# Kernel tuning notes

Measured on AMD Instinct MI355X. Metric: run time of the kernel, lower is better.

The kernel has to match this reference:

```python
import jax, jax.numpy as jnp
import numpy as np

N_NODES = 50000
N_EDGES = 800000
D_FEAT = 128
HIDDEN = 128
BERT_DIM = 768
BATCH = 4096
MAX_ENT = 20
COMB = BERT_DIM + HIDDEN  # 896


def setup_inputs() -> dict:
    key = jax.random.key(0)
    ks = jax.random.split(key, 12)
    article_bert_embeddings = jax.random.normal(ks[0], (BATCH, BERT_DIM), dtype=jnp.float32)
    x = jax.random.normal(ks[1], (N_NODES, D_FEAT), dtype=jnp.float32)
    edge_index = jax.random.randint(ks[2], (2, N_EDGES), 0, N_NODES, dtype=jnp.int64)
    entity_map = jax.random.randint(ks[3], (BATCH, MAX_ENT), 0, N_NODES, dtype=jnp.int64)
    pad = jax.random.uniform(ks[4], (BATCH, MAX_ENT)) < 0.3
    entity_map = jnp.where(pad, jnp.int64(-1), entity_map)
    s = 1.0 / np.sqrt(D_FEAT)
    W1 = jax.random.normal(ks[5], (D_FEAT, HIDDEN), dtype=jnp.float32) * s
    b1 = jnp.zeros((HIDDEN,), dtype=jnp.float32)
    W2 = jax.random.normal(ks[6], (HIDDEN, HIDDEN), dtype=jnp.float32) * (1.0 / np.sqrt(HIDDEN))
    b2 = jnp.zeros((HIDDEN,), dtype=jnp.float32)
    fc1_w = jax.random.normal(ks[7], (COMB, COMB // 2), dtype=jnp.float32) * (1.0 / np.sqrt(COMB))
    fc1_b = jnp.zeros((COMB // 2,), dtype=jnp.float32)
    fc2_w = jax.random.normal(ks[8], (COMB // 2, 1), dtype=jnp.float32) * (1.0 / np.sqrt(COMB // 2))
    fc2_b = jnp.zeros((1,), dtype=jnp.float32)
    return dict(article_bert_embeddings=article_bert_embeddings, x=x,
                edge_index=edge_index, entity_map=entity_map,
                W1=W1, b1=b1, W2=W2, b2=b2,
                fc1_w=fc1_w, fc1_b=fc1_b, fc2_w=fc2_w, fc2_b=fc2_b)


def _gcn_norm(edge_index, n_nodes):
    # add self loops (PyG GCNConv default) and compute symmetric normalization
    loops = jnp.arange(n_nodes, dtype=edge_index.dtype)
    src = jnp.concatenate([edge_index[0], loops])
    dst = jnp.concatenate([edge_index[1], loops])
    deg = jax.ops.segment_sum(jnp.ones_like(dst, dtype=jnp.float32), dst, num_segments=n_nodes)
    dinv = jnp.where(deg > 0, jax.lax.rsqrt(deg), 0.0)
    norm = dinv[src] * dinv[dst]  # [E+N]
    return src, dst, norm


def _gcn_conv(h, W, b, src, dst, norm, n_nodes):
    h = h @ W                                   # [N, H] transform first (cheaper)
    msg = h[src] * norm[:, None]                # [E+N, H] gather
    out = jax.ops.segment_sum(msg, dst, num_segments=n_nodes)
    return out + b


def reference(article_bert_embeddings, x, edge_index, entity_map,
              W1, b1, W2, b2, fc1_w, fc1_b, fc2_w, fc2_b):
    n = x.shape[0]
    src, dst, norm = _gcn_norm(edge_index, n)
    # GNN (dropout in eval mode = identity)
    h = jax.nn.relu(_gcn_conv(x, W1, b1, src, dst, norm, n))
    h = jax.nn.relu(_gcn_conv(h, W2, b2, src, dst, norm, n))
    # ragged mean over entity lists (-1 = padding), fully vectorized
    mask = entity_map >= 0                           # [B, M]
    safe_ids = jnp.where(mask, entity_map, 0)
    gathered = h[safe_ids] * mask[..., None]         # [B, M, H]
    cnt = jnp.maximum(mask.sum(axis=1, keepdims=True).astype(h.dtype), 1.0)
    batch_gnn = gathered.sum(axis=1) / cnt           # [B, H]; rows w/ no entities stay 0
    combined = jnp.concatenate([article_bert_embeddings, batch_gnn], axis=1)
    z = jax.nn.relu(combined @ fc1_w + fc1_b)
    logits = z @ fc2_w + fc2_b
    return jax.nn.sigmoid(logits)
```

## Files before the change

### kernel.cpp

```cpp
#include <hip/hip_runtime.h>
#include <math.h>

typedef __bf16 bf16_t;
typedef __bf16 bfrag8 __attribute__((ext_vector_type(8)));
typedef float  facc4  __attribute__((ext_vector_type(4)));
typedef float  f32x2  __attribute__((ext_vector_type(2)));

#define NBUCK 512
#define BCAP  4096
#define BINCH 2048

__device__ inline unsigned short f2b(float x) {
    unsigned int u = __float_as_uint(x);
    unsigned int r = (u + 0x7fffu + ((u >> 16) & 1u)) >> 16;
    return (unsigned short)r;
}
__device__ inline unsigned int pack2(float lo, float hi) {
    return (unsigned int)f2b(lo) | ((unsigned int)f2b(hi) << 16);
}
__device__ inline float blo(unsigned int q) { return __uint_as_float(q << 16); }
__device__ inline float bhi(unsigned int q) { return __uint_as_float(q & 0xffff0000u); }

#if __has_builtin(__builtin_amdgcn_cvt_pk_f32_fp8) && __has_builtin(__builtin_amdgcn_cvt_pk_fp8_f32)
#define HW_FP8 1
#endif

__device__ inline f32x2 fp8pair_dec(unsigned short v) {
#ifdef HW_FP8
    return __builtin_amdgcn_cvt_pk_f32_fp8((int)(unsigned int)v, false);
#else
    f32x2 r;
    unsigned char b0 = (unsigned char)(v & 0xff), b1 = (unsigned char)(v >> 8);
    {
        int e = (b0 >> 3) & 0xf, m = b0 & 7;
        float mag = e ? ldexpf(8.f + m, e - 10) : ldexpf((float)m, -9);
        r.x = (b0 & 0x80) ? -mag : mag;
    }
    {
        int e = (b1 >> 3) & 0xf, m = b1 & 7;
        float mag = e ? ldexpf(8.f + m, e - 10) : ldexpf((float)m, -9);
        r.y = (b1 & 0x80) ? -mag : mag;
    }
    return r;
#endif
}
__device__ inline unsigned char fp8_enc(float x) {
#ifdef HW_FP8
    return (unsigned char)(__builtin_amdgcn_cvt_pk_fp8_f32(x, x, 0, false) & 0xff);
#else
    unsigned char s = (x < 0.f) ? 0x80 : 0;
    float ax = fabsf(x);
    if (!(ax > 0.f)) return s;
    if (ax >= 448.f) return s | 0x7e;
    if (ax < 0.015625f) {
        int q = (int)rintf(ax * 512.f);
        return s | (unsigned char)q;
    }
    int e; float m = frexpf(ax, &e);
    int q = (int)rintf(m * 16.f);
    int E = e - 1;
    if (q == 16) { q = 8; ++E; }
    if (E > 8) return s | 0x7e;
    return s | (unsigned char)(((E + 7) << 3) | (q - 8));
#endif
}

__device__ inline int bucket_of(int d, int N) {
    return (int)(((long long)d * NBUCK) / N);
}


__device__ inline void bin2_body(char* smem, const int* __restrict__ src,
                                 const int* __restrict__ dst,
                                 int* __restrict__ bcnt,
                                 unsigned int* __restrict__ ebuf,
                                 int E, int N, int bb) {
    unsigned int* sorted = (unsigned int*)smem;
    int* hist   = (int*)(smem + 16384);
    int* lstart = (int*)(smem + 18432);
    int* gbase  = (int*)(smem + 20480);
    int* sm     = (int*)(smem + 22528);
    int tid = threadIdx.x;
    int base = bb * BINCH;
    int cnt = min(BINCH, E - base);
    hist[tid] = 0; hist[tid + 256] = 0;
    __syncthreads();
    unsigned int mye[8]; int myb[8];
#pragma unroll
    for (int i = 0; i < 8; ++i) {
        int idx = i * 256 + tid;
        myb[i] = -1;
        if (idx < cnt) {
            int e = base + idx;
            int s = src[e], d = dst[e];
            mye[i] = ((unsigned int)s << 16) | (unsigned int)d;
            int b = bucket_of(d, N);
            myb[i] = b;
            atomicAdd(&hist[b], 1);
        }
    }
    __syncthreads();
    int p0 = hist[2 * tid], p1 = hist[2 * tid + 1];
    sm[tid] = p0 + p1;
    __syncthreads();
    for (int off = 1; off < 256; off <<= 1) {
        int x = (tid >= off) ? sm[tid - off] : 0;
        __syncthreads();
        sm[tid] += x;
        __syncthreads();
    }
    int excl = sm[tid] - (p0 + p1);
    lstart[2 * tid] = excl;
    lstart[2 * tid + 1] = excl + p0;
    __syncthreads();
    hist[tid] = lstart[tid]; hist[tid + 256] = lstart[tid + 256];
    __syncthreads();
#pragma unroll
    for (int i = 0; i < 8; ++i) {
        if (myb[i] >= 0) {
            int pos = atomicAdd(&hist[myb[i]], 1);
            sorted[pos] = mye[i];
        }
    }
    __syncthreads();
    for (int b = tid; b < NBUCK; b += 256) {
        int c = hist[b] - lstart[b];
        gbase[b] = (c > 0) ? atomicAdd(&bcnt[b], c) : 0;
    }
    __syncthreads();
    for (int idx = tid; idx < cnt; idx += 256) {
        unsigned int v = sorted[idx];
        int b = bucket_of((int)(v & 0xffffu), N);
        ebuf[(size_t)b * BCAP + gbase[b] + (idx - lstart[b])] = v;
    }
}

__device__ inline void build2_body(char* smem, const unsigned int* __restrict__ ebuf,
                                   const int* __restrict__ bcnt,
                                   int* __restrict__ offs,
                                   float* __restrict__ dinv,
                                   unsigned short* __restrict__ csr,
                                   int N, int E, int b) {
    unsigned short* seg = (unsigned short*)smem;
    int* cnt_l  = (int*)(smem + 8192);
    int* scan_l = (int*)(smem + 8704);
    int* curs   = (int*)(smem + 9216);
    int* smr    = (int*)(smem + 9728);
    int tid = threadIdx.x;
    int part = 0;
    for (int j = tid; j < b; j += 256) part += bcnt[j];
    smr[tid] = part;
    __syncthreads();
    for (int off = 128; off > 0; off >>= 1) {
        if (tid < off) smr[tid] += smr[tid + off];
        __syncthreads();
    }
    int base = smr[0];
    int lo = (int)(((long long)b * N + NBUCK - 1) / NBUCK);
    int cnt = bcnt[b];
    int nrange = (int)(((long long)(b + 1) * N + NBUCK - 1) / NBUCK) - lo;
    if (b == 0 && tid == 0) offs[N] = E;
    if (tid < 128) cnt_l[tid] = 0;
    __syncthreads();
    for (int i = tid; i < cnt; i += 256) {
        unsigned int v = ebuf[(size_t)b * BCAP + i];
        atomicAdd(&cnt_l[(int)(v & 0xffffu) - lo], 1);
    }
    __syncthreads();
    if (tid < 128) scan_l[tid] = cnt_l[tid];
    __syncthreads();
    for (int off = 1; off < 128; off <<= 1) {
        int x = 0;
        if (tid < 128 && tid >= off) x = scan_l[tid - off];
        __syncthreads();
        if (tid < 128) scan_l[tid] += x;
        __syncthreads();
    }
    if (tid < 128) {
        int excl = scan_l[tid] - cnt_l[tid];
        curs[tid] = excl;
        if (tid < nrange) {
            offs[lo + tid] = base + excl;
            dinv[lo + tid] = rsqrtf((float)(cnt_l[tid] + 1));
        }
    }
    __syncthreads();
    for (int i = tid; i < cnt; i += 256) {
        unsigned int v = ebuf[(size_t)b * BCAP + i];
        int d = (int)(v & 0xffffu) - lo;
        int p = atomicAdd(&curs[d], 1);
        seg[p] = (unsigned short)(v >> 16);
    }
    __syncthreads();
    for (int i = tid; i < cnt; i += 256) csr[base + i] = seg[i];
}

__device__ inline void gemm1_body(char* smem, const float* __restrict__ A,
                                  const bf16_t* __restrict__ Bt,
                                  unsigned char* __restrict__ out8, int M, int bb) {
    bf16_t* As = (bf16_t*)smem;
    bf16_t* Bs = (bf16_t*)(smem + 17408);
    int t = threadIdx.x;
    int wave = t >> 6, lane = t & 63, quad = lane >> 4, l16 = lane & 15;
    int r0 = bb * 64;
#pragma unroll
    for (int i = 0; i < 4; ++i) {
        int chunk = t + i * 256;
        int row = chunk >> 4, c8 = (chunk & 15) << 3;
        int gr = r0 + row;
        float4 a0 = make_float4(0.f, 0.f, 0.f, 0.f), a1 = a0;
        if (gr < M) {
            a0 = *(const float4*)&A[(size_t)gr * 128 + c8];
            a1 = *(const float4*)&A[(size_t)gr * 128 + c8 + 4];
        }
        *(uint4*)&As[row * 136 + c8] =
            make_uint4(pack2(a0.x, a0.y), pack2(a0.z, a0.w),
                       pack2(a1.x, a1.y), pack2(a1.z, a1.w));
    }
#pragma unroll
    for (int i = 0; i < 8; ++i) {
        int chunk = t + i * 256;
        int row = chunk >> 4, c8 = (chunk & 15) << 3;
        *(uint4*)&Bs[row * 136 + c8] = *(const uint4*)&Bt[row * 128 + c8];
    }
    __syncthreads();

    facc4 acc[8];
#pragma unroll
    for (int nt = 0; nt < 8; ++nt) acc[nt] = (facc4){0.f, 0.f, 0.f, 0.f};
    int arow = (wave << 4) + l16;
#pragma unroll
    for (int ks = 0; ks < 4; ++ks) {
        int kk = ks * 32 + quad * 8;
        bfrag8 af = *(const bfrag8*)&As[arow * 136 + kk];
#pragma unroll
        for (int nt = 0; nt < 8; ++nt) {
            bfrag8 bf = *(const bfrag8*)&Bs[(nt * 16 + l16) * 136 + kk];
            acc[nt] = __builtin_amdgcn_mfma_f32_16x16x32_bf16(af, bf, acc[nt], 0, 0, 0);
        }
    }
    __syncthreads();
    unsigned char* f8t = (unsigned char*)As;
    int wrow0 = (wave << 4) + quad * 4;
#pragma unroll
    for (int r = 0; r < 4; ++r) {
        int row = wrow0 + r;
#pragma unroll
        for (int nt = 0; nt < 8; ++nt)
            f8t[row * 128 + nt * 16 + l16] = fp8_enc(acc[nt][r]);
    }
    __syncthreads();
#pragma unroll
    for (int i = 0; i < 2; ++i) {
        int idx = t + i * 256;
        int row = idx >> 3, cc = (idx & 7) << 4;
        int gr = r0 + row;
        if (gr < M) *(uint4*)&out8[(size_t)gr * 128 + cc] = *(const uint4*)&f8t[row * 128 + cc];
    }
}

__global__ __launch_bounds__(256) void k_bin_gemm(const int* __restrict__ src,
                                                  const int* __restrict__ dst,
                                                  int* __restrict__ bcnt,
                                                  unsigned int* __restrict__ ebuf,
                                                  int E, int N,
                                                  const float* __restrict__ A,
                                                  const bf16_t* __restrict__ Bt,
                                                  unsigned char* __restrict__ out8,
                                                  int nbin) {
    __shared__ __align__(16) char smem[52224];
    if ((int)blockIdx.x < nbin)
        bin2_body(smem, src, dst, bcnt, ebuf, E, N, blockIdx.x);
    else
        gemm1_body(smem, A, Bt, out8, N, blockIdx.x - nbin);
}

__global__ __launch_bounds__(256) void k_build_gemm(const unsigned int* __restrict__ ebuf,
                                                    const int* __restrict__ bcnt,
                                                    int* __restrict__ offs,
                                                    float* __restrict__ dinv,
                                                    unsigned short* __restrict__ csr,
                                                    int N, int E,
                                                    const float* __restrict__ A,
                                                    const bf16_t* __restrict__ Bt,
                                                    unsigned char* __restrict__ out8,
                                                    int tile0) {
    __shared__ __align__(16) char smem[52224];
    if ((int)blockIdx.x < NBUCK)
        build2_body(smem, ebuf, bcnt, offs, dinv, csr, N, E, blockIdx.x);
    else
        gemm1_body(smem, A, Bt, out8, N, blockIdx.x - NBUCK + tile0);
}

__global__ __launch_bounds__(256) void k_prep(const float* __restrict__ bert,
                                              unsigned int* __restrict__ bertb, int n8,
                                              const float* __restrict__ W1,
                                              unsigned short* __restrict__ w1t,
                                              const float* __restrict__ W2,
                                              unsigned short* __restrict__ w2t,
                                              const float* __restrict__ Wf,
                                              unsigned short* __restrict__ fwt,
                                              int* __restrict__ bcnt,
                                              float* __restrict__ logacc) {
    __shared__ float tile[64][65];
    int ncvt = (n8 + 255) / 256;
    int bb = blockIdx.x, tid = threadIdx.x;
    if (bb < ncvt) {
        int i = bb * 256 + tid;
        if (i >= n8) return;
        const float4* p = (const float4*)bert + (size_t)i * 2;
        float4 a = p[0], b = p[1];
        uint4 o;
        o.x = pack2(a.x, a.y);
        o.y = pack2(a.z, a.w);
        o.z = pack2(b.x, b.y);
        o.w = pack2(b.z, b.w);
        ((uint4*)bertb)[i] = o;
        return;
    }
    bb -= ncvt;
    if (bb < 128) {
        int i = bb * 256 + tid;
        const float* W = (i < 16384) ? W1 : W2;
        unsigned short* Wt = (i < 16384) ? w1t : w2t;
        int idx = i & 16383;
        int n = idx >> 7, k = idx & 127;
        Wt[idx] = f2b(W[k * 128 + n]);
        return;
    }
    bb -= 128;
    if (bb < 98) {
        int n0 = (bb % 7) * 64, k0 = (bb / 7) * 64;
#pragma unroll
        for (int i = 0; i < 16; ++i) {
            int idx = i * 256 + tid;
            int r = idx >> 6, c = idx & 63;
            tile[r][c] = Wf[(size_t)(k0 + r) * 448 + n0 + c];
        }
        __syncthreads();
#pragma unroll
        for (int i = 0; i < 16; ++i) {
            int idx = i * 256 + tid;
            int c = idx >> 6, r = idx & 63;
            fwt[(size_t)(n0 + c) * 896 + k0 + r] = f2b(tile[r][c]);
        }
        return;
    }
    if (tid < 256) { bcnt[tid] = 0; bcnt[tid + 256] = 0; }
#pragma unroll
    for (int i = 0; i < 16; ++i) logacc[i * 256 + tid] = 0.f;
}

__global__ __launch_bounds__(256) void k_gemm_nn128(const bf16_t* __restrict__ A,
                                                    const bf16_t* __restrict__ Bt,
                                                    const float* __restrict__ rs,
                                                    unsigned char* __restrict__ out8, int M) {
    __shared__ bf16_t As[64 * 136];
    __shared__ bf16_t Bs[128 * 136];
    int t = threadIdx.x;
    int wave = t >> 6, lane = t & 63, quad = lane >> 4, l16 = lane & 15;
    int r0 = blockIdx.x * 64;
#pragma unroll
    for (int i = 0; i < 4; ++i) {
        int chunk = t + i * 256;
        int row = chunk >> 4, c8 = (chunk & 15) << 3;
        int gr = r0 + row;
        uint4 v = make_uint4(0u, 0u, 0u, 0u);
        if (gr < M) v = *(const uint4*)&A[(size_t)gr * 128 + c8];
        *(uint4*)&As[row * 136 + c8] = v;
    }
#pragma unroll
    for (int i = 0; i < 8; ++i) {
        int chunk = t + i * 256;
        int row = chunk >> 4, c8 = (chunk & 15) << 3;
        *(uint4*)&Bs[row * 136 + c8] = *(const uint4*)&Bt[row * 128 + c8];
    }
    __syncthreads();

    facc4 acc[8];
#pragma unroll
    for (int nt = 0; nt < 8; ++nt) acc[nt] = (facc4){0.f, 0.f, 0.f, 0.f};
    int arow = (wave << 4) + l16;
#pragma unroll
    for (int ks = 0; ks < 4; ++ks) {
        int kk = ks * 32 + quad * 8;
        bfrag8 af = *(const bfrag8*)&As[arow * 136 + kk];
#pragma unroll
        for (int nt = 0; nt < 8; ++nt) {
            bfrag8 bf = *(const bfrag8*)&Bs[(nt * 16 + l16) * 136 + kk];
            acc[nt] = __builtin_amdgcn_mfma_f32_16x16x32_bf16(af, bf, acc[nt], 0, 0, 0);
        }
    }
    __syncthreads();
    unsigned char* f8t = (unsigned char*)As;
    int wrow0 = (wave << 4) + quad * 4;
#pragma unroll
    for (int r = 0; r < 4; ++r) {
        int row = wrow0 + r;
        float sc = rs[min(r0 + row, M - 1)];
#pragma unroll
        for (int nt = 0; nt < 8; ++nt)
            f8t[row * 128 + nt * 16 + l16] = fp8_enc(acc[nt][r] * sc);
    }
    __syncthreads();
#pragma unroll
    for (int i = 0; i < 2; ++i) {
        int idx = t + i * 256;
        int row = idx >> 3, cc = (idx & 7) << 4;
        int gr = r0 + row;
        if (gr < M) *(uint4*)&out8[(size_t)gr * 128 + cc] = *(const uint4*)&f8t[row * 128 + cc];
    }
}

__global__ __launch_bounds__(256) void k_agg_w(const unsigned short* __restrict__ hx8,
                                               const unsigned short* __restrict__ csr,
                                               const int* __restrict__ offs,
                                               const float* __restrict__ dinv,
                                               const float* __restrict__ bias,
                                               unsigned int* __restrict__ out, int N) {
    int node = blockIdx.x * 4 + (threadIdx.x >> 6);
    int lane = threadIdx.x & 63;
    if (node >= N) return;
    float di = dinv[node];
    f32x2 sf = fp8pair_dec(hx8[(size_t)node * 64 + lane]);
    float acc0 = sf.x * di, acc1 = sf.y * di;
    int s0 = offs[node], s1 = offs[node + 1];
    for (int base = s0; base < s1; base += 64) {
        int nloc = min(64, s1 - base);
        int en = 0; float dvl = 0.f;
        if (lane < nloc) { en = (int)csr[base + lane]; dvl = dinv[en]; }
        int j = 0;
        for (; j + 16 <= nloc; j += 16) {
            int sid[16]; float dv[16]; unsigned short g[16];
#pragma unroll
            for (int u = 0; u < 16; ++u) {
                sid[u] = __shfl(en, j + u, 64);
                dv[u]  = __shfl(dvl, j + u, 64);
            }
#pragma unroll
            for (int u = 0; u < 16; ++u) g[u] = hx8[(size_t)sid[u] * 64 + lane];
#pragma unroll
            for (int u = 0; u < 16; ++u) {
                f32x2 d = fp8pair_dec(g[u]);
                acc0 += d.x * dv[u]; acc1 += d.y * dv[u];
            }
        }
        for (; j + 4 <= nloc; j += 4) {
            int sid[4]; float dv[4]; unsigned short g[4];
#pragma unroll
            for (int u = 0; u < 4; ++u) {
                sid[u] = __shfl(en, j + u, 64);
                dv[u]  = __shfl(dvl, j + u, 64);
            }
#pragma unroll
            for (int u = 0; u < 4; ++u) g[u] = hx8[(size_t)sid[u] * 64 + lane];
#pragma unroll
            for (int u = 0; u < 4; ++u) {
                f32x2 d = fp8pair_dec(g[u]);
                acc0 += d.x * dv[u]; acc1 += d.y * dv[u];
            }
        }
        for (; j < nloc; ++j) {
            int srcn = __shfl(en, j, 64);
            float dv = __shfl(dvl, j, 64);
            f32x2 d = fp8pair_dec(hx8[(size_t)srcn * 64 + lane]);
            acc0 += d.x * dv; acc1 += d.y * dv;
        }
    }
    float2 bb = *(const float2*)&bias[lane * 2];
    float v0 = fmaxf(acc0 * di + bb.x, 0.f);
    float v1 = fmaxf(acc1 * di + bb.y, 0.f);
    out[(size_t)node * 64 + lane] = pack2(v0, v1);
}

__global__ __launch_bounds__(256) void k_agg_b(const unsigned short* __restrict__ hx8,
                                               const unsigned short* __restrict__ csr,
                                               const int* __restrict__ offs,
                                               const float* __restrict__ dinv,
                                               const float* __restrict__ bias,
                                               unsigned int* __restrict__ out, int N) {
    int node = blockIdx.x * 4 + (threadIdx.x >> 6);
    int lane = threadIdx.x & 63;
    if (node >= N) return;
    float di = dinv[node];
    f32x2 sf = fp8pair_dec(hx8[(size_t)node * 64 + lane]);
    float acc0 = sf.x, acc1 = sf.y;
    int s0 = offs[node], s1 = offs[node + 1];
    for (int base = s0; base < s1; base += 64) {
        int nloc = min(64, s1 - base);
        int en = 0;
        if (lane < nloc) en = (int)csr[base + lane];
        int j = 0;
        for (; j + 16 <= nloc; j += 16) {
            int sid[16]; unsigned short g[16];
#pragma unroll
            for (int u = 0; u < 16; ++u) sid[u] = __shfl(en, j + u, 64);
#pragma unroll
            for (int u = 0; u < 16; ++u) g[u] = hx8[(size_t)sid[u] * 64 + lane];
#pragma unroll
            for (int u = 0; u < 16; ++u) { f32x2 d = fp8pair_dec(g[u]); acc0 += d.x; acc1 += d.y; }
        }
        for (; j + 4 <= nloc; j += 4) {
            int sid[4]; unsigned short g[4];
#pragma unroll
            for (int u = 0; u < 4; ++u) sid[u] = __shfl(en, j + u, 64);
#pragma unroll
            for (int u = 0; u < 4; ++u) g[u] = hx8[(size_t)sid[u] * 64 + lane];
#pragma unroll
            for (int u = 0; u < 4; ++u) { f32x2 d = fp8pair_dec(g[u]); acc0 += d.x; acc1 += d.y; }
        }
        for (; j < nloc; ++j) {
            int srcn = __shfl(en, j, 64);
            f32x2 d = fp8pair_dec(hx8[(size_t)srcn * 64 + lane]);
            acc0 += d.x; acc1 += d.y;
        }
    }
    float2 bb = *(const float2*)&bias[lane * 2];
    float v0 = fmaxf(acc0 * di + bb.x, 0.f);
    float v1 = fmaxf(acc1 * di + bb.y, 0.f);
    out[(size_t)node * 64 + lane] = pack2(v0, v1);
}

__global__ __launch_bounds__(256) void k_pool_b(const unsigned int* __restrict__ h,
                                                const int* __restrict__ ent,
                                                unsigned int* __restrict__ out) {
    int r = blockIdx.x * 4 + (threadIdx.x >> 6);
    int lane = threadIdx.x & 63;
    float a0 = 0.f, a1 = 0.f;
    int cnt = 0;
#pragma unroll
    for (int m = 0; m < 20; ++m) {
        int id = ent[r * 20 + m];
        if (id >= 0) {
            unsigned int q = h[(size_t)id * 64 + lane];
            a0 += blo(q); a1 += bhi(q); cnt++;
        }
    }
    float inv = 1.f / (float)max(cnt, 1);
    out[(size_t)r * 64 + lane] = pack2(a0 * inv, a1 * inv);
}

__global__ __launch_bounds__(256) void k_mlp1_mfma(const bf16_t* __restrict__ bertb,
                                                   const bf16_t* __restrict__ gnnb,
                                                   const bf16_t* __restrict__ fwt,
                                                   const float* __restrict__ fb,
                                                   const float* __restrict__ w2,
                                                   float* __restrict__ logacc) {
    __shared__ bf16_t As[64 * 136];
    __shared__ bf16_t Bs[64 * 136];
    int t = threadIdx.x;
    int wave = t >> 6, lane = t & 63, quad = lane >> 4, l16 = lane & 15;
    int r0 = blockIdx.x * 64, c0 = blockIdx.y * 64;
    facc4 acc[4];
#pragma unroll
    for (int nt = 0; nt < 4; ++nt) acc[nt] = (facc4){0.f, 0.f, 0.f, 0.f};

    for (int ks = 0; ks < 7; ++ks) {
#pragma unroll
        for (int i = 0; i < 4; ++i) {
            int chunk = t + i * 256;
            int row = chunk >> 4, c8 = (chunk & 15) << 3;
            int gr = r0 + row;
            const bf16_t* srcp = (ks < 6) ? &bertb[(size_t)gr * 768 + ks * 128 + c8]
                                          : &gnnb[(size_t)gr * 128 + c8];
            *(uint4*)&As[row * 136 + c8] = *(const uint4*)srcp;
        }
#pragma unroll
        for (int i = 0; i < 4; ++i) {
            int chunk = t + i * 256;
            int row = chunk >> 4, c8 = (chunk & 15) << 3;
            *(uint4*)&Bs[row * 136 + c8] =
                *(const uint4*)&fwt[(size_t)(c0 + row) * 896 + ks * 128 + c8];
        }
        __syncthreads();
        int arow = (wave << 4) + l16;
#pragma unroll
        for (int sub = 0; sub < 4; ++sub) {
            int kk = sub * 32 + quad * 8;
            bfrag8 af = *(const bfrag8*)&As[arow * 136 + kk];
#pragma unroll
            for (int nt = 0; nt < 4; ++nt) {
                bfrag8 bf = *(const bfrag8*)&Bs[(nt * 16 + l16) * 136 + kk];
                acc[nt] = __builtin_amdgcn_mfma_f32_16x16x32_bf16(af, bf, acc[nt], 0, 0, 0);
            }
        }
        __syncthreads();
    }
    int rbase = r0 + (wave << 4) + quad * 4;
    float part[4] = {0.f, 0.f, 0.f, 0.f};
#pragma unroll
    for (int nt = 0; nt < 4; ++nt) {
        int col = c0 + nt * 16 + l16;
        float bb = fb[col];
        float ww = w2[col];
#pragma unroll
        for (int r = 0; r < 4; ++r)
            part[r] += fmaxf(acc[nt][r] + bb, 0.f) * ww;
    }
#pragma unroll
    for (int m = 8; m >= 1; m >>= 1) {
#pragma unroll
        for (int r = 0; r < 4; ++r) part[r] += __shfl_xor(part[r], m, 64);
    }
    if (l16 == 0) {
#pragma unroll
        for (int r = 0; r < 4; ++r) atomicAdd(&logacc[rbase + r], part[r]);
    }
}

__global__ void k_sig(const float* __restrict__ logacc, const float* __restrict__ b,
                      float* __restrict__ out, int B) {
    int i = blockIdx.x * 256 + threadIdx.x;
    if (i < B) out[i] = 1.f / (1.f + expf(-(logacc[i] + b[0])));
}

extern "C" void kernel_launch(void* const* d_in, const int* in_sizes, int n_in,
                              void* d_out, int out_size, void* d_ws, size_t ws_size,
                              hipStream_t stream) {
    const float* bert = (const float*)d_in[0];
    const float* x    = (const float*)d_in[1];
    const int*   ei   = (const int*)d_in[2];
    const int*   ent  = (const int*)d_in[3];
    const float* W1   = (const float*)d_in[4];
    const float* b1   = (const float*)d_in[5];
    const float* W2   = (const float*)d_in[6];
    const float* b2   = (const float*)d_in[7];
    const float* fc1w = (const float*)d_in[8];
    const float* fc1b = (const float*)d_in[9];
    const float* fc2w = (const float*)d_in[10];
    const float* fc2b = (const float*)d_in[11];
    float* out = (float*)d_out;

    const int N = in_sizes[1] / 128;
    const int E = in_sizes[2] / 2;
    const int B = in_sizes[0] / 768;

    const int* srcv = ei;
    const int* dstv = ei + E;

    char* wsp = (char*)d_ws;
    size_t off = 0;
    auto alloc = [&](size_t bytes) -> void* {
        void* p = wsp + off;
        off += (bytes + 255) & ~(size_t)255;
        return p;
    };
    float* dinv   = (float*)alloc((size_t)N * 4);
    int*   offs   = (int*)alloc((size_t)(N + 1) * 4);
    int*   bcnt   = (int*)alloc(NBUCK * 4);
    float* logacc = (float*)alloc((size_t)B * 4);
    unsigned int*   ebuf  = (unsigned int*)alloc((size_t)NBUCK * BCAP * 4);
    unsigned short* csr16 = (unsigned short*)alloc((size_t)E * 2);
    bf16_t* bertb = (bf16_t*)alloc((size_t)B * 768 * 2);
    bf16_t* w1t   = (bf16_t*)alloc(128 * 128 * 2);
    bf16_t* w2t   = (bf16_t*)alloc(128 * 128 * 2);
    bf16_t* fwt   = (bf16_t*)alloc((size_t)896 * 448 * 2);
    unsigned char* g8a = (unsigned char*)alloc((size_t)N * 128);
    unsigned char* g8b = (unsigned char*)alloc((size_t)N * 128);
    bf16_t* hbuf  = (bf16_t*)alloc((size_t)N * 128 * 2);
    bf16_t* gnnb  = (bf16_t*)alloc((size_t)B * 128 * 2);
    (void)ws_size; (void)n_in; (void)out_size;

    int nb8 = B * 768 / 8;
    int ncvt = (nb8 + 255) / 256;
    int nprep = ncvt + 128 + 98 + 1;
    int nbin = (E + BINCH - 1) / BINCH;
    int gb = (N + 63) / 64;
    int g1a = gb / 2, g1b = gb - g1a;

    k_prep<<<nprep, 256, 0, stream>>>(bert, (unsigned int*)bertb, nb8,
                                      W1, (unsigned short*)w1t, W2, (unsigned short*)w2t,
                                      fc1w, (unsigned short*)fwt, bcnt, logacc);
    k_bin_gemm<<<nbin + g1a, 256, 0, stream>>>(srcv, dstv, bcnt, ebuf, E, N,
                                               x, w1t, g8a, nbin);
    k_build_gemm<<<NBUCK + g1b, 256, 0, stream>>>(ebuf, bcnt, offs, dinv, csr16, N, E,
                                                  x, w1t, g8a, g1a);
    k_agg_w<<<(N + 3) / 4, 256, 0, stream>>>((const unsigned short*)g8a, csr16, offs, dinv, b1,
                                             (unsigned int*)hbuf, N);
    k_gemm_nn128<<<gb, 256, 0, stream>>>(hbuf, w2t, dinv, g8b, N);
    k_agg_b<<<(N + 3) / 4, 256, 0, stream>>>((const unsigned short*)g8b, csr16, offs, dinv, b2,
                                             (unsigned int*)hbuf, N);
    k_pool_b<<<B / 4, 256, 0, stream>>>((const unsigned int*)hbuf, ent, (unsigned int*)gnnb);
    k_mlp1_mfma<<<dim3(B / 64, 7), 256, 0, stream>>>(bertb, gnnb, fwt, fc1b, fc2w, logacc);
    k_sig<<<(B + 255) / 256, 256, 0, stream>>>(logacc, fc2b, out, B);
}
```

Before: 214.9 us.

## Process four nodes per wave in aggregation, prescale layer-1 features, halve GEMM LDS

Unifies the two aggregation kernels into one that handles four destination nodes per wave and interleaves their neighbor gathers to raise memory-level parallelism. Layer-1 source scaling by dinv moves into a separate pass that rewrites the fp8 features in place. The GEMMs now load the weight matrix in two 64-row halves, which cuts shared memory per block to allow higher occupancy. The changes add an extra kernel pass, a second fp8 rounding, and wasted iterations when the four nodes' degrees differ.

```diff
diff --git a/kernel.cpp b/kernel.cpp
--- a/kernel.cpp
+++ b/kernel.cpp
@@ -9,6 +9,7 @@
 #define NBUCK 512
 #define BCAP  4096
 #define BINCH 2048
+#define KN 4
 
 __device__ inline unsigned short f2b(float x) {
     unsigned int u = __float_as_uint(x);
@@ -217,37 +218,39 @@
             make_uint4(pack2(a0.x, a0.y), pack2(a0.z, a0.w),
                        pack2(a1.x, a1.y), pack2(a1.z, a1.w));
     }
-#pragma unroll
-    for (int i = 0; i < 8; ++i) {
-        int chunk = t + i * 256;
-        int row = chunk >> 4, c8 = (chunk & 15) << 3;
-        *(uint4*)&Bs[row * 136 + c8] = *(const uint4*)&Bt[row * 128 + c8];
-    }
-    __syncthreads();
-
     facc4 acc[8];
 #pragma unroll
     for (int nt = 0; nt < 8; ++nt) acc[nt] = (facc4){0.f, 0.f, 0.f, 0.f};
     int arow = (wave << 4) + l16;
 #pragma unroll
-    for (int ks = 0; ks < 4; ++ks) {
-        int kk = ks * 32 + quad * 8;
-        bfrag8 af = *(const bfrag8*)&As[arow * 136 + kk];
-#pragma unroll
-        for (int nt = 0; nt < 8; ++nt) {
-            bfrag8 bf = *(const bfrag8*)&Bs[(nt * 16 + l16) * 136 + kk];
-            acc[nt] = __builtin_amdgcn_mfma_f32_16x16x32_bf16(af, bf, acc[nt], 0, 0, 0);
-        }
-    }
-    __syncthreads();
+    for (int h = 0; h < 2; ++h) {
+#pragma unroll
+        for (int i = 0; i < 4; ++i) {
+            int chunk = t + i * 256;
+            int row = chunk >> 4, c8 = (chunk & 15) << 3;
+            *(uint4*)&Bs[row * 136 + c8] = *(const uint4*)&Bt[(h * 64 + row) * 128 + c8];
+        }
+        __syncthreads();
+#pragma unroll
+        for (int ks = 0; ks < 4; ++ks) {
+            int kk = ks * 32 + quad * 8;
+            bfrag8 af = *(const bfrag8*)&As[arow * 136 + kk];
+#pragma unroll
+            for (int nt = 0; nt < 4; ++nt) {
+                bfrag8 bf = *(const bfrag8*)&Bs[(nt * 16 + l16) * 136 + kk];
+                acc[h * 4 + nt] = __builtin_amdgcn_mfma_f32_16x16x32_bf16(af, bf, acc[h * 4 + nt], 0, 0, 0);
+            }
+        }
+        __syncthreads();
+    }
     unsigned char* f8t = (unsigned char*)As;
     int wrow0 = (wave << 4) + quad * 4;
 #pragma unroll
     for (int r = 0; r < 4; ++r) {
         int row = wrow0 + r;
 #pragma unroll
-        for (int nt = 0; nt < 8; ++nt)
-            f8t[row * 128 + nt * 16 + l16] = fp8_enc(acc[nt][r]);
+        for (int nt2 = 0; nt2 < 8; ++nt2)
+            f8t[row * 128 + (nt2 >> 2) * 64 + (nt2 & 3) * 16 + l16] = fp8_enc(acc[nt2][r]);
     }
     __syncthreads();
 #pragma unroll
@@ -268,7 +271,7 @@
                                                   const bf16_t* __restrict__ Bt,
                                                   unsigned char* __restrict__ out8,
                                                   int nbin) {
-    __shared__ __align__(16) char smem[52224];
+    __shared__ __align__(16) char smem[34816];
     if ((int)blockIdx.x < nbin)
         bin2_body(smem, src, dst, bcnt, ebuf, E, N, blockIdx.x);
     else
@@ -285,7 +288,7 @@
                                                     const bf16_t* __restrict__ Bt,
                                                     unsigned char* __restrict__ out8,
                                                     int tile0) {
-    __shared__ __align__(16) char smem[52224];
+    __shared__ __align__(16) char smem[34816];
     if ((int)blockIdx.x < NBUCK)
         build2_body(smem, ebuf, bcnt, offs, dinv, csr, N, E, blockIdx.x);
     else
@@ -351,12 +354,35 @@
     for (int i = 0; i < 16; ++i) logacc[i * 256 + tid] = 0.f;
 }
 
+__global__ __launch_bounds__(256) void k_scale8(unsigned int* __restrict__ g8,
+                                                const float* __restrict__ dinv, int N) {
+    int i = blockIdx.x * 256 + threadIdx.x;
+    int total = N * 8;
+    if (i >= total) return;
+    int row = i >> 3;
+    float d = dinv[row];
+    uint4 v = ((const uint4*)g8)[i];
+    unsigned int w[4] = {v.x, v.y, v.z, v.w};
+#pragma unroll
+    for (int q = 0; q < 4; ++q) {
+        unsigned int x = w[q], y = 0;
+#pragma unroll
+        for (int h = 0; h < 2; ++h) {
+            f32x2 p = fp8pair_dec((unsigned short)(x >> (h * 16)));
+            y |= (unsigned int)fp8_enc(p.x * d) << (h * 16);
+            y |= (unsigned int)fp8_enc(p.y * d) << (h * 16 + 8);
+        }
+        w[q] = y;
+    }
+    ((uint4*)g8)[i] = make_uint4(w[0], w[1], w[2], w[3]);
+}
+
 __global__ __launch_bounds__(256) void k_gemm_nn128(const bf16_t* __restrict__ A,
                                                     const bf16_t* __restrict__ Bt,
                                                     const float* __restrict__ rs,
                                                     unsigned char* __restrict__ out8, int M) {
     __shared__ bf16_t As[64 * 136];
-    __shared__ bf16_t Bs[128 * 136];
+    __shared__ bf16_t Bs[64 * 136];
     int t = threadIdx.x;
     int wave = t >> 6, lane = t & 63, quad = lane >> 4, l16 = lane & 15;
     int r0 = blockIdx.x * 64;
@@ -369,29 +395,31 @@
         if (gr < M) v = *(const uint4*)&A[(size_t)gr * 128 + c8];
         *(uint4*)&As[row * 136 + c8] = v;
     }
-#pragma unroll
-    for (int i = 0; i < 8; ++i) {
-        int chunk = t + i * 256;
-        int row = chunk >> 4, c8 = (chunk & 15) << 3;
-        *(uint4*)&Bs[row * 136 + c8] = *(const uint4*)&Bt[row * 128 + c8];
-    }
-    __syncthreads();
-
     facc4 acc[8];
 #pragma unroll
     for (int nt = 0; nt < 8; ++nt) acc[nt] = (facc4){0.f, 0.f, 0.f, 0.f};
     int arow = (wave << 4) + l16;
 #pragma unroll
-    for (int ks = 0; ks < 4; ++ks) {
-        int kk = ks * 32 + quad * 8;
-        bfrag8 af = *(const bfrag8*)&As[arow * 136 + kk];
-#pragma unroll
-        for (int nt = 0; nt < 8; ++nt) {
-            bfrag8 bf = *(const bfrag8*)&Bs[(nt * 16 + l16) * 136 + kk];
-            acc[nt] = __builtin_amdgcn_mfma_f32_16x16x32_bf16(af, bf, acc[nt], 0, 0, 0);
-        }
-    }
-    __syncthreads();
+    for (int h = 0; h < 2; ++h) {
+#pragma unroll
+        for (int i = 0; i < 4; ++i) {
+            int chunk = t + i * 256;
+            int row = chunk >> 4, c8 = (chunk & 15) << 3;
+            *(uint4*)&Bs[row * 136 + c8] = *(const uint4*)&Bt[(h * 64 + row) * 128 + c8];
+        }
+        __syncthreads();
+#pragma unroll
+        for (int ks = 0; ks < 4; ++ks) {
+            int kk = ks * 32 + quad * 8;
+            bfrag8 af = *(const bfrag8*)&As[arow * 136 + kk];
+#pragma unroll
+            for (int nt = 0; nt < 4; ++nt) {
+                bfrag8 bf = *(const bfrag8*)&Bs[(nt * 16 + l16) * 136 + kk];
+                acc[h * 4 + nt] = __builtin_amdgcn_mfma_f32_16x16x32_bf16(af, bf, acc[h * 4 + nt], 0, 0, 0);
+            }
+        }
+        __syncthreads();
+    }
     unsigned char* f8t = (unsigned char*)As;
     int wrow0 = (wave << 4) + quad * 4;
 #pragma unroll
@@ -399,8 +427,8 @@
         int row = wrow0 + r;
         float sc = rs[min(r0 + row, M - 1)];
 #pragma unroll
-        for (int nt = 0; nt < 8; ++nt)
-            f8t[row * 128 + nt * 16 + l16] = fp8_enc(acc[nt][r] * sc);
+        for (int nt2 = 0; nt2 < 8; ++nt2)
+            f8t[row * 128 + (nt2 >> 2) * 64 + (nt2 & 3) * 16 + l16] = fp8_enc(acc[nt2][r] * sc);
     }
     __syncthreads();
 #pragma unroll
@@ -412,113 +440,77 @@
     }
 }
 
-__global__ __launch_bounds__(256) void k_agg_w(const unsigned short* __restrict__ hx8,
+__global__ __launch_bounds__(256) void k_agg_p(const unsigned short* __restrict__ hx8,
                                                const unsigned short* __restrict__ csr,
                                                const int* __restrict__ offs,
                                                const float* __restrict__ dinv,
                                                const float* __restrict__ bias,
                                                unsigned int* __restrict__ out, int N) {
-    int node = blockIdx.x * 4 + (threadIdx.x >> 6);
-    int lane = threadIdx.x & 63;
-    if (node >= N) return;
-    float di = dinv[node];
-    f32x2 sf = fp8pair_dec(hx8[(size_t)node * 64 + lane]);
-    float acc0 = sf.x * di, acc1 = sf.y * di;
-    int s0 = offs[node], s1 = offs[node + 1];
-    for (int base = s0; base < s1; base += 64) {
-        int nloc = min(64, s1 - base);
-        int en = 0; float dvl = 0.f;
-        if (lane < nloc) { en = (int)csr[base + lane]; dvl = dinv[en]; }
-        int j = 0;
-        for (; j + 16 <= nloc; j += 16) {
-            int sid[16]; float dv[16]; unsigned short g[16];
-#pragma unroll
-            for (int u = 0; u < 16; ++u) {
-                sid[u] = __shfl(en, j + u, 64);
-                dv[u]  = __shfl(dvl, j + u, 64);
+    int t = threadIdx.x, wv = t >> 6, lane = t & 63;
+    int nb = (blockIdx.x * 4 + wv) * KN;
+    if (nb >= N) return;
+    float a0[KN], a1[KN], di[KN];
+    int s0[KN], dg[KN];
+#pragma unroll
+    for (int k = 0; k < KN; ++k) {
+        int nd = nb + k;
+        if (nd < N) {
+            f32x2 s = fp8pair_dec(hx8[(size_t)nd * 64 + lane]);
+            a0[k] = s.x; a1[k] = s.y;
+            s0[k] = offs[nd];
+            dg[k] = offs[nd + 1] - s0[k];
+            di[k] = dinv[nd];
+        } else { a0[k] = a1[k] = 0.f; s0[k] = 0; dg[k] = 0; di[k] = 0.f; }
+    }
+    int maxd = 0;
+#pragma unroll
+    for (int k = 0; k < KN; ++k) maxd = max(maxd, dg[k]);
+    for (int eb = 0; eb < maxd; eb += 64) {
+        int en[KN];
+#pragma unroll
+        for (int k = 0; k < KN; ++k) {
+            int nl = dg[k] - eb;
+            en[k] = 0;
+            if (nl > 0 && lane < nl) en[k] = (int)csr[s0[k] + eb + lane];
+        }
+        for (int j = 0; j < 64; j += 8) {
+            unsigned short g[KN][8];
+            bool any = false;
+#pragma unroll
+            for (int k = 0; k < KN; ++k) {
+                int nl = dg[k] - eb; if (nl > 64) nl = 64;
+                if (j < nl) {
+                    any = true;
+#pragma unroll
+                    for (int u = 0; u < 8; ++u) {
+                        int sid = __shfl(en[k], j + u, 64);
+                        g[k][u] = (j + u < nl) ? hx8[(size_t)sid * 64 + lane] : (unsigned short)0;
+                    }
+                } else {
+#pragma unroll
+                    for (int u = 0; u < 8; ++u) g[k][u] = 0;
+                }
             }
-#pragma unroll
-            for (int u = 0; u < 16; ++u) g[u] = hx8[(size_t)sid[u] * 64 + lane];
-#pragma unroll
-            for (int u = 0; u < 16; ++u) {
-                f32x2 d = fp8pair_dec(g[u]);
-                acc0 += d.x * dv[u]; acc1 += d.y * dv[u];
-            }
-        }
-        for (; j + 4 <= nloc; j += 4) {
-            int sid[4]; float dv[4]; unsigned short g[4];
-#pragma unroll
-            for (int u = 0; u < 4; ++u) {
-                sid[u] = __shfl(en, j + u, 64);
-                dv[u]  = __shfl(dvl, j + u, 64);
-            }
-#pragma unroll
-            for (int u = 0; u < 4; ++u) g[u] = hx8[(size_t)sid[u] * 64 + lane];
-#pragma unroll
-            for (int u = 0; u < 4; ++u) {
-                f32x2 d = fp8pair_dec(g[u]);
-                acc0 += d.x * dv[u]; acc1 += d.y * dv[u];
-            }
-        }
-        for (; j < nloc; ++j) {
-            int srcn = __shfl(en, j, 64);
-            float dv = __shfl(dvl, j, 64);
-            f32x2 d = fp8pair_dec(hx8[(size_t)srcn * 64 + lane]);
-            acc0 += d.x * dv; acc1 += d.y * dv;
+            if (!any) break;
+#pragma unroll
+            for (int k = 0; k < KN; ++k)
+#pragma unroll
+                for (int u = 0; u < 8; ++u) {
+                    f32x2 d = fp8pair_dec(g[k][u]);
+                    a0[k] += d.x; a1[k] += d.y;
+                }
         }
     }
     float2 bb = *(const float2*)&bias[lane * 2];
-    float v0 = fmaxf(acc0 * di + bb.x, 0.f);
-    float v1 = fmaxf(acc1 * di + bb.y, 0.f);
-    out[(size_t)node * 64 + lane] = pack2(v0, v1);
-}
-
-__global__ __launch_bounds__(256) void k_agg_b(const unsigned short* __restrict__ hx8,
-                                               const unsigned short* __restrict__ csr,
-                                               const int* __restrict__ offs,
-                                               const float* __restrict__ dinv,
-                                               const float* __restrict__ bias,
-                                               unsigned int* __restrict__ out, int N) {
-    int node = blockIdx.x * 4 + (threadIdx.x >> 6);
-    int lane = threadIdx.x & 63;
-    if (node >= N) return;
-    float di = dinv[node];
-    f32x2 sf = fp8pair_dec(hx8[(size_t)node * 64 + lane]);
-    float acc0 = sf.x, acc1 = sf.y;
-    int s0 = offs[node], s1 = offs[node + 1];
-    for (int base = s0; base < s1; base += 64) {
-        int nloc = min(64, s1 - base);
-        int en = 0;
-        if (lane < nloc) en = (int)csr[base + lane];
-        int j = 0;
-        for (; j + 16 <= nloc; j += 16) {
-            int sid[16]; unsigned short g[16];
-#pragma unroll
-            for (int u = 0; u < 16; ++u) sid[u] = __shfl(en, j + u, 64);
-#pragma unroll
-            for (int u = 0; u < 16; ++u) g[u] = hx8[(size_t)sid[u] * 64 + lane];
-#pragma unroll
-            for (int u = 0; u < 16; ++u) { f32x2 d = fp8pair_dec(g[u]); acc0 += d.x; acc1 += d.y; }
-        }
-        for (; j + 4 <= nloc; j += 4) {
-            int sid[4]; unsigned short g[4];
-#pragma unroll
-            for (int u = 0; u < 4; ++u) sid[u] = __shfl(en, j + u, 64);
-#pragma unroll
-            for (int u = 0; u < 4; ++u) g[u] = hx8[(size_t)sid[u] * 64 + lane];
-#pragma unroll
-            for (int u = 0; u < 4; ++u) { f32x2 d = fp8pair_dec(g[u]); acc0 += d.x; acc1 += d.y; }
-        }
-        for (; j < nloc; ++j) {
-            int srcn = __shfl(en, j, 64);
-            f32x2 d = fp8pair_dec(hx8[(size_t)srcn * 64 + lane]);
-            acc0 += d.x; acc1 += d.y;
-        }
-    }
-    float2 bb = *(const float2*)&bias[lane * 2];
-    float v0 = fmaxf(acc0 * di + bb.x, 0.f);
-    float v1 = fmaxf(acc1 * di + bb.y, 0.f);
-    out[(size_t)node * 64 + lane] = pack2(v0, v1);
+#pragma unroll
+    for (int k = 0; k < KN; ++k) {
+        int nd = nb + k;
+        if (nd < N) {
+            float v0 = fmaxf(a0[k] * di[k] + bb.x, 0.f);
+            float v1 = fmaxf(a1[k] * di[k] + bb.y, 0.f);
+            out[(size_t)nd * 64 + lane] = pack2(v0, v1);
+        }
+    }
 }
 
 __global__ __launch_bounds__(256) void k_pool_b(const unsigned int* __restrict__ h,
@@ -675,11 +667,12 @@
                                                x, w1t, g8a, nbin);
     k_build_gemm<<<NBUCK + g1b, 256, 0, stream>>>(ebuf, bcnt, offs, dinv, csr16, N, E,
                                                   x, w1t, g8a, g1a);
-    k_agg_w<<<(N + 3) / 4, 256, 0, stream>>>((const unsigned short*)g8a, csr16, offs, dinv, b1,
-                                             (unsigned int*)hbuf, N);
+    k_scale8<<<(N * 8 + 255) / 256, 256, 0, stream>>>((unsigned int*)g8a, dinv, N);
+    k_agg_p<<<(N + 4 * KN * 4 - 1) / (4 * KN), 256, 0, stream>>>(
+        (const unsigned short*)g8a, csr16, offs, dinv, b1, (unsigned int*)hbuf, N);
     k_gemm_nn128<<<gb, 256, 0, stream>>>(hbuf, w2t, dinv, g8b, N);
-    k_agg_b<<<(N + 3) / 4, 256, 0, stream>>>((const unsigned short*)g8b, csr16, offs, dinv, b2,
-                                             (unsigned int*)hbuf, N);
+    k_agg_p<<<(N + 4 * KN * 4 - 1) / (4 * KN), 256, 0, stream>>>(
+        (const unsigned short*)g8b, csr16, offs, dinv, b2, (unsigned int*)hbuf, N);
     k_pool_b<<<B / 4, 256, 0, stream>>>((const unsigned int*)hbuf, ent, (unsigned int*)gnnb);
     k_mlp1_mfma<<<dim3(B / 64, 7), 256, 0, stream>>>(bertb, gnnb, fwt, fc1b, fc2w, logacc);
     k_sig<<<(B + 255) / 256, 256, 0, stream>>>(logacc, fc2b, out, B);
```

Result: slower. 225.1 us (+4.8%).
